# Performance work log

Hardware: AMD Instinct MI355X
Metric: run time of the kernel (lower is better)

Reference implementation:

```python
import jax, jax.numpy as jnp
import numpy as np

B, N, K, IN_C, OUT_C = 8, 20000, 9, 64, 64


def setup_inputs() -> dict:
    key = jax.random.key(0)
    k1, k2, k3, k4, k5, k6 = jax.random.split(key, 6)
    x = jax.random.normal(k1, (B, N, IN_C), dtype=jnp.float32)
    neighbor_index = jax.random.randint(k2, (B, N, K), 0, N, dtype=jnp.int64)
    # adjweight initialized to identity per original code (eye expanded over num_pts)
    adjweight = jnp.broadcast_to(jnp.eye(K, dtype=jnp.float32), (N, K, K))
    # conv: Linear(in_c*K -> out_c); mlp_out: Linear(in_c -> out_c)
    conv_w = jax.random.normal(k3, (OUT_C, IN_C * K), dtype=jnp.float32) / np.sqrt(IN_C * K)
    conv_b = jax.random.normal(k4, (OUT_C,), dtype=jnp.float32) * 0.01
    mlp_w = jax.random.normal(k5, (OUT_C, IN_C), dtype=jnp.float32) / np.sqrt(IN_C)
    mlp_b = jax.random.normal(k6, (OUT_C,), dtype=jnp.float32) * 0.01
    return {"x": x, "neighbor_index": neighbor_index, "adjweight": adjweight,
            "conv_w": conv_w, "conv_b": conv_b, "mlp_w": mlp_w, "mlp_b": mlp_b}


def reference(x, neighbor_index, adjweight, conv_w, conv_b, mlp_w, mlp_b):
    bsize, num_pts, feats = x.shape
    num_neighbor = neighbor_index.shape[-1]
    # zero_padding mask: last point zeroed
    mask = jnp.ones((1, num_pts, 1), dtype=x.dtype).at[0, -1, 0].set(0.0)
    x = x * mask
    # per-batch gather of neighbor features: [B, N, K, F]
    x_neighbors = jax.vmap(lambda xb, ib: xb[ib])(x, neighbor_index)
    # learnable per-point KxK mixing over the neighbor dim: bnkf,nkt->bntf
    x_neighbors = jnp.einsum('bnkf,nkt->bntf', x_neighbors, adjweight)
    x_neighbors = jax.nn.elu(x_neighbors).reshape(bsize, num_pts, num_neighbor * feats)
    out_feat = jax.nn.elu(x_neighbors @ conv_w.T + conv_b) * mask
    x_res = x @ mlp_w.T + mlp_b
    return out_feat + x_res
```

## Files before the change

kernel.cpp:

```cpp
#include <hip/hip_runtime.h>

#define BB 8
#define NN 20000
#define KK 9
#define KC 576
#define ROWS (BB*NN)

#define WST_ELE   36864
#define WST2_ELE  4096
#define XB_ELE    (ROWS*64)
#define WST_OFF   0
#define WST2_OFF  36864
#define XB_OFF    40960

#define PSTRIDE 584

typedef __bf16 bf16x8 __attribute__((ext_vector_type(8)));
typedef float  f32x4  __attribute__((ext_vector_type(4)));
typedef unsigned short u16x8 __attribute__((ext_vector_type(8)));

__device__ __forceinline__ unsigned short f2bf(float f) {
    unsigned u = __builtin_bit_cast(unsigned, f);
    u += 0x7FFFu + ((u >> 16) & 1u);
    return (unsigned short)(u >> 16);
}
__device__ __forceinline__ float bf2f(unsigned short h) {
    return __builtin_bit_cast(float, ((unsigned)h) << 16);
}
__device__ __forceinline__ float elu_f(float v) { return v > 0.0f ? v : (__expf(v) - 1.0f); }

__global__ void __launch_bounds__(256) paiconv_prep(
        const float* __restrict__ x,
        const float* __restrict__ conv_w,
        const float* __restrict__ mlp_w,
        unsigned short* __restrict__ ws16) {
    const int tid = blockIdx.x * 256 + threadIdx.x;

    if (tid < XB_ELE / 8) {
        const int e = tid * 8;
        const int r = e >> 6;
        const int n = r % NN;
        u16x8 pk;
        if (n == NN - 1) {
            #pragma unroll
            for (int i = 0; i < 8; ++i) pk[i] = 0;
        } else {
            f32x4 lo = *(const f32x4*)(x + e);
            f32x4 hi = *(const f32x4*)(x + e + 4);
            #pragma unroll
            for (int i = 0; i < 4; ++i) { pk[i] = f2bf(lo[i]); pk[4 + i] = f2bf(hi[i]); }
        }
        *(u16x8*)(ws16 + XB_OFF + e) = pk;
    }
    if (tid < WST_ELE) {
        const int kk = tid & 31, o = (tid >> 5) & 63, mch = tid >> 11;
        const int c = mch / 9, t = mch - 9 * c;
        ws16[WST_OFF + tid] = f2bf(conv_w[o * KC + t * 64 + c * 32 + kk]);
    }
    if (tid < WST2_ELE) {
        const int kk = tid & 31, o = (tid >> 5) & 63, c2 = tid >> 11;
        ws16[WST2_OFF + tid] = f2bf(mlp_w[o * 64 + c2 * 32 + kk]);
    }
}

__global__ void __launch_bounds__(128, 2) paiconv_main(
        const int*   __restrict__ nidx,
        const float* __restrict__ adj,
        const float* __restrict__ conv_b,
        const float* __restrict__ mlp_b,
        const unsigned short* __restrict__ ws16,
        float* __restrict__ out) {
    __shared__ unsigned short P[2][16 * PSTRIDE];

    const int tx   = threadIdx.x;
    const int lane = tx & 63;
    const int l15  = lane & 15;
    const int q    = lane >> 4;
    const int wave = __builtin_amdgcn_readfirstlane(tx >> 6);
    const int batch = blockIdx.x & 7;
    const int chunk = blockIdx.x >> 3;
    const int n0    = chunk * 32 + wave * 16;
    const int rowbase = batch * NN + n0;

    const unsigned short* Wst  = ws16 + WST_OFF;
    const unsigned short* Wst2 = ws16 + WST2_OFF;
    const unsigned short* XB   = ws16 + XB_OFF;
    const unsigned short* XBb  = XB + (size_t)batch * NN * 64;
    unsigned short* Pw = &P[wave][0];

    #pragma unroll 2
    for (int r = 0; r < 16; ++r) {
        const int n    = n0 + r;
        const int grow = rowbase + r;
        const float* adjrow = adj + (size_t)n * 81;

        float vf[KK];
        #pragma unroll
        for (int k = 0; k < KK; ++k) {
            const int idx = __builtin_amdgcn_readfirstlane(nidx[grow * KK + k]);
            const unsigned short* rp = XBb + idx * 64;
            vf[k] = bf2f(rp[lane]);
        }
        float m[KK] = {0.f,0.f,0.f,0.f,0.f,0.f,0.f,0.f,0.f};
        #pragma unroll
        for (int k = 0; k < KK; ++k) {
            #pragma unroll
            for (int t = 0; t < KK; ++t)
                m[t] = __builtin_fmaf(adjrow[k * 9 + t], vf[k], m[t]);
        }
        #pragma unroll
        for (int t = 0; t < KK; ++t)
            Pw[r * PSTRIDE + t * 64 + lane] = f2bf(elu_f(m[t]));
    }

    f32x4 acc[4];
    f32x4 acc2[4];
    #pragma unroll
    for (int ot = 0; ot < 4; ++ot) { acc[ot] = (f32x4)0.0f; acc2[ot] = (f32x4)0.0f; }

    #pragma unroll
    for (int c = 0; c < 2; ++c) {
        #pragma unroll
        for (int t = 0; t < KK; ++t) {
            const u16x8* ap = (const u16x8*)(Pw + l15 * PSTRIDE + t * 64 + c * 32 + q * 8);
            bf16x8 afrag = __builtin_bit_cast(bf16x8, *ap);
            const int mch = c * 9 + t;
            #pragma unroll
            for (int ot = 0; ot < 4; ++ot) {
                const u16x8* wp = (const u16x8*)(Wst + mch * 2048 + (ot * 16 + l15) * 32 + q * 8);
                bf16x8 bfrag = __builtin_bit_cast(bf16x8, *wp);
                acc[ot] = __builtin_amdgcn_mfma_f32_16x16x32_bf16(afrag, bfrag, acc[ot], 0, 0, 0);
            }
        }
    }

    #pragma unroll
    for (int c2 = 0; c2 < 2; ++c2) {
        bf16x8 a2 = *(const bf16x8*)(XB + (size_t)(rowbase + l15) * 64 + c2 * 32 + q * 8);
        #pragma unroll
        for (int ot = 0; ot < 4; ++ot) {
            const u16x8* wp = (const u16x8*)(Wst2 + c2 * 2048 + (ot * 16 + l15) * 32 + q * 8);
            bf16x8 b2 = __builtin_bit_cast(bf16x8, *wp);
            acc2[ot] = __builtin_amdgcn_mfma_f32_16x16x32_bf16(a2, b2, acc2[ot], 0, 0, 0);
        }
    }

    float* smf = (float*)Pw;
    #pragma unroll
    for (int ot = 0; ot < 4; ++ot) {
        const int o = ot * 16 + l15;
        const float cb = conv_b[o];
        const float mb = mlp_b[o];
        #pragma unroll
        for (int i = 0; i < 4; ++i) {
            const int rr = 4 * q + i;
            float f = elu_f(acc[ot][i] + cb);
            if (n0 + rr == NN - 1) f = 0.0f;
            f += acc2[ot][i] + mb;
            smf[rr * 68 + o] = f;
        }
    }
    #pragma unroll
    for (int p = 0; p < 4; ++p) {
        const int r = p * 4 + q;
        f32x4 vv = *(const f32x4*)&smf[r * 68 + l15 * 4];
        *(f32x4*)(out + (size_t)(rowbase + r) * 64 + l15 * 4) = vv;
    }
}

extern "C" void kernel_launch(void* const* d_in, const int* in_sizes, int n_in,
                              void* d_out, int out_size, void* d_ws, size_t ws_size,
                              hipStream_t stream) {
    const float* x      = (const float*)d_in[0];
    const int*   nidx   = (const int*)  d_in[1];
    const float* adj    = (const float*)d_in[2];
    const float* conv_w = (const float*)d_in[3];
    const float* conv_b = (const float*)d_in[4];
    const float* mlp_w  = (const float*)d_in[5];
    const float* mlp_b  = (const float*)d_in[6];
    unsigned short* ws16 = (unsigned short*)d_ws;
    float* out = (float*)d_out;

    const int prep_blocks = (XB_ELE / 8) / 256;
    paiconv_prep<<<prep_blocks, 256, 0, stream>>>(x, conv_w, mlp_w, ws16);

    const int main_blocks = 8 * 625;
    paiconv_main<<<main_blocks, 128, 0, stream>>>(nidx, adj, conv_b, mlp_b, ws16, out);
}
```

Before: 252.7 us.

## Prefetch neighbor gathers in 4-row groups and XOR-swizzle LDS tile

Restructures the gather phase so each wave loads neighbor features for four rows at once and prefetches the next group's gathers while computing the current group's KxK mixing. This overlaps gather latency with compute. The padded LDS stride is replaced by an XOR swizzle on 16-byte columns to avoid bank conflicts without padding. The readfirstlane on indices is dropped and the 2-waves-per-SIMD launch bound hint is removed, which raises register pressure and risks lower occupancy.

```diff
diff --git a/kernel.cpp b/kernel.cpp
--- a/kernel.cpp
+++ b/kernel.cpp
@@ -13,7 +13,7 @@
 #define WST2_OFF  36864
 #define XB_OFF    40960
 
-#define PSTRIDE 584
+#define PROW 576
 
 typedef __bf16 bf16x8 __attribute__((ext_vector_type(8)));
 typedef float  f32x4  __attribute__((ext_vector_type(4)));
@@ -63,14 +63,14 @@
     }
 }
 
-__global__ void __launch_bounds__(128, 2) paiconv_main(
+__global__ void __launch_bounds__(128) paiconv_main(
         const int*   __restrict__ nidx,
         const float* __restrict__ adj,
         const float* __restrict__ conv_b,
         const float* __restrict__ mlp_b,
         const unsigned short* __restrict__ ws16,
         float* __restrict__ out) {
-    __shared__ unsigned short P[2][16 * PSTRIDE];
+    __shared__ unsigned short P[2][16 * PROW];
 
     const int tx   = threadIdx.x;
     const int lane = tx & 63;
@@ -88,29 +88,59 @@
     const unsigned short* XBb  = XB + (size_t)batch * NN * 64;
     unsigned short* Pw = &P[wave][0];
 
-    #pragma unroll 2
-    for (int r = 0; r < 16; ++r) {
-        const int n    = n0 + r;
-        const int grow = rowbase + r;
-        const float* adjrow = adj + (size_t)n * 81;
-
-        float vf[KK];
+    const int wcol_lane = lane >> 3;
+    const int wsub      = lane & 7;
+
+    float vf[4][KK];
+    #pragma unroll
+    for (int rr = 0; rr < 4; ++rr) {
+        const int grow = rowbase + rr;
         #pragma unroll
         for (int k = 0; k < KK; ++k) {
-            const int idx = __builtin_amdgcn_readfirstlane(nidx[grow * KK + k]);
-            const unsigned short* rp = XBb + idx * 64;
-            vf[k] = bf2f(rp[lane]);
-        }
-        float m[KK] = {0.f,0.f,0.f,0.f,0.f,0.f,0.f,0.f,0.f};
-        #pragma unroll
-        for (int k = 0; k < KK; ++k) {
-            #pragma unroll
-            for (int t = 0; t < KK; ++t)
-                m[t] = __builtin_fmaf(adjrow[k * 9 + t], vf[k], m[t]);
-        }
-        #pragma unroll
-        for (int t = 0; t < KK; ++t)
-            Pw[r * PSTRIDE + t * 64 + lane] = f2bf(elu_f(m[t]));
+            const int idx = nidx[grow * KK + k];
+            vf[rr][k] = bf2f(XBb[idx * 64 + lane]);
+        }
+    }
+
+    #pragma unroll
+    for (int rg = 0; rg < 4; ++rg) {
+        float vn[4][KK];
+        if (rg < 3) {
+            #pragma unroll
+            for (int rr = 0; rr < 4; ++rr) {
+                const int grow = rowbase + (rg + 1) * 4 + rr;
+                #pragma unroll
+                for (int k = 0; k < KK; ++k) {
+                    const int idx = nidx[grow * KK + k];
+                    vn[rr][k] = bf2f(XBb[idx * 64 + lane]);
+                }
+            }
+        }
+        #pragma unroll
+        for (int rr = 0; rr < 4; ++rr) {
+            const int r = rg * 4 + rr;
+            const float* adjrow = adj + (size_t)(n0 + r) * 81;
+            float m[KK] = {0.f,0.f,0.f,0.f,0.f,0.f,0.f,0.f,0.f};
+            #pragma unroll
+            for (int k = 0; k < KK; ++k) {
+                const float a0 = vf[rr][k];
+                #pragma unroll
+                for (int t = 0; t < KK; ++t)
+                    m[t] = __builtin_fmaf(adjrow[k * 9 + t], a0, m[t]);
+            }
+            const int rx = r & 7;
+            #pragma unroll
+            for (int t = 0; t < KK; ++t) {
+                const int colu = (t * 8 + wcol_lane) ^ rx;
+                Pw[r * PROW + colu * 8 + wsub] = f2bf(elu_f(m[t]));
+            }
+        }
+        if (rg < 3) {
+            #pragma unroll
+            for (int rr = 0; rr < 4; ++rr)
+                #pragma unroll
+                for (int k = 0; k < KK; ++k) vf[rr][k] = vn[rr][k];
+        }
     }
 
     f32x4 acc[4];
@@ -118,11 +148,13 @@
     #pragma unroll
     for (int ot = 0; ot < 4; ++ot) { acc[ot] = (f32x4)0.0f; acc2[ot] = (f32x4)0.0f; }
 
+    const int lx = l15 & 7;
     #pragma unroll
     for (int c = 0; c < 2; ++c) {
         #pragma unroll
         for (int t = 0; t < KK; ++t) {
-            const u16x8* ap = (const u16x8*)(Pw + l15 * PSTRIDE + t * 64 + c * 32 + q * 8);
+            const int colu = (t * 8 + c * 4 + q) ^ lx;
+            const u16x8* ap = (const u16x8*)(Pw + l15 * PROW + colu * 8);
             bf16x8 afrag = __builtin_bit_cast(bf16x8, *ap);
             const int mch = c * 9 + t;
             #pragma unroll
```

After: 273.6 us. 8.3% more time.
